# Performance work log

Measured on AMD Instinct MI355X. Metric: run time of the kernel, lower is better.

Reference implementation:

```python
import jax, jax.numpy as jnp
import numpy as np

N_NODES = 100000
N_EDGES = 1600000
N_GRAPHS = 256
F_IN = 54


def setup_inputs() -> dict:
    key = jax.random.key(0)
    ks = jax.random.split(key, 16)
    x = jax.random.normal(ks[0], (N_NODES, F_IN), dtype=jnp.float32)
    edge_index = jax.random.randint(ks[1], (2, N_EDGES), 0, N_NODES, dtype=jnp.int32)
    batch = jnp.sort(jax.random.randint(ks[2], (N_NODES,), 0, N_GRAPHS, dtype=jnp.int32))

    def lin(k, fi, fo):
        kw, kb = jax.random.split(k)
        lim = 1.0 / np.sqrt(fi)
        W = jax.random.uniform(kw, (fi, fo), minval=-lim, maxval=lim, dtype=jnp.float32)
        b = jax.random.uniform(kb, (fo,), minval=-lim, maxval=lim, dtype=jnp.float32)
        return W, b

    W1, b1 = lin(ks[3], 54, 54)
    W2, b2 = lin(ks[4], 54, 108)
    W3, b3 = lin(ks[5], 108, 216)
    Wf1, bf1 = lin(ks[6], 216, 1024)
    Wf2, bf2 = lin(ks[7], 1024, 128)
    return {"x": x, "edge_index": edge_index, "batch": batch,
            "W1": W1, "b1": b1, "W2": W2, "b2": b2, "W3": W3, "b3": b3,
            "Wf1": Wf1, "bf1": bf1, "Wf2": Wf2, "bf2": bf2}


def _gcn_norm(edge_index, n):
    # add self-loops, symmetric degree normalization (PyG GCNConv default)
    loop = jnp.arange(n, dtype=edge_index.dtype)
    row = jnp.concatenate([edge_index[0], loop])
    col = jnp.concatenate([edge_index[1], loop])
    deg = jax.ops.segment_sum(jnp.ones_like(col, dtype=jnp.float32), col, num_segments=n)
    dinv = jnp.where(deg > 0, jax.lax.rsqrt(deg), 0.0)
    norm = dinv[row] * dinv[col]
    return row, col, norm


def _gcn_conv(x, row, col, norm, W, b, n):
    h = x @ W                                  # [N, Fout]
    msg = h[row] * norm[:, None]               # [E+N, Fout] gather + scale
    out = jax.ops.segment_sum(msg, col, num_segments=n)  # scatter-add
    return out + b


def reference(x, edge_index, batch, W1, b1, W2, b2, W3, b3, Wf1, bf1, Wf2, bf2):
    n = x.shape[0]
    row, col, norm = _gcn_norm(edge_index, n)
    h = jax.nn.relu(_gcn_conv(x, row, col, norm, W1, b1, n))
    h = jax.nn.relu(_gcn_conv(h, row, col, norm, W2, b2, n))
    h = jax.nn.relu(_gcn_conv(h, row, col, norm, W3, b3, n))
    # global mean pool per graph
    sums = jax.ops.segment_sum(h, batch, num_segments=N_GRAPHS)
    cnts = jax.ops.segment_sum(jnp.ones((n,), jnp.float32), batch, num_segments=N_GRAPHS)
    pooled = sums / jnp.maximum(cnts, 1.0)[:, None]   # [G, 216]
    g = jax.nn.relu(pooled @ Wf1 + bf1)               # dropout = identity (eval)
    return g @ Wf2 + bf2                              # [G, 128]
```

## Files before the change

### kernel.cpp

```cpp
#include <hip/hip_runtime.h>


typedef _Float16 f16;
typedef _Float16 f16x2 __attribute__((ext_vector_type(2)));
typedef _Float16 f16x8 __attribute__((ext_vector_type(8)));
typedef float f32x4 __attribute__((ext_vector_type(4)));

static __host__ __device__ inline int cdiv(int a, int b) { return (a + b - 1) / b; }

constexpr int BSPAN = 512;
constexpr int EPB   = 4096;
constexpr int EPT   = EPB / 256;

template <int V>
__device__ __forceinline__ void vload(float* d, const float* s) {
    if constexpr (V == 1) { d[0] = s[0]; }
    else if constexpr (V == 2) { float2 t = *reinterpret_cast<const float2*>(s); d[0] = t.x; d[1] = t.y; }
    else { float4 t = *reinterpret_cast<const float4*>(s); d[0] = t.x; d[1] = t.y; d[2] = t.z; d[3] = t.w; }
}

__device__ __forceinline__ void wpack_one(const float* W, f16* Wb, int K, int F,
                                          int KT, int idx) {
    int j = idx & 7;
    int lane = (idx >> 3) & 63;
    int fi = idx >> 9;
    int kt = fi % KT;
    int nt = fi / KT;
    int k = kt * 32 + (lane >> 4) * 8 + j;
    int nn = nt * 16 + (lane & 15);
    Wb[idx] = (k < K && nn < F) ? (f16)W[k * F + nn] : (f16)0.f;
}

__global__ void k_init(const int* __restrict__ batch, int* __restrict__ start,
                       float* __restrict__ psum, int* __restrict__ bktCnt,
                       int* __restrict__ bktCur,
                       const float* __restrict__ W1, const float* __restrict__ W2,
                       const float* __restrict__ W3, f16* __restrict__ w1b,
                       f16* __restrict__ w2b, f16* __restrict__ w3b,
                       int n, int g) {
    int i = blockIdx.x * blockDim.x + threadIdx.x;
    if (i < g * 216) psum[i] = 0.f;
    if (i < 256) { bktCnt[i] = 0; bktCur[i] = 0; }
    constexpr int T1 = 4 * 2 * 512;
    constexpr int T2 = 7 * 2 * 512;
    constexpr int T3 = 14 * 4 * 512;
    if (i < T1) wpack_one(W1, w1b, 54, 54, 2, i);
    else if (i < T1 + T2) wpack_one(W2, w2b, 54, 108, 2, i - T1);
    else if (i < T1 + T2 + T3) wpack_one(W3, w3b, 108, 216, 4, i - T1 - T2);
    if (i < n) {
        int b = batch[i];
        int bp = (i == 0) ? -1 : batch[i - 1];
        for (int gg = bp + 1; gg <= b; gg++) start[gg] = i;
        if (i == n - 1)
            for (int gg = b + 1; gg <= g; gg++) start[gg] = n;
    }
}

__global__ __launch_bounds__(256) void k_bkt_hist(const int* __restrict__ col,
                                                  int* bktCnt, int e, int nb) {
    __shared__ int hist[256];
    int t = threadIdx.x;
    hist[t] = 0;
    __syncthreads();
    int base = blockIdx.x * EPB;
#pragma unroll
    for (int j = 0; j < EPT; j++) {
        int idx = base + j * 256 + t;
        if (idx < e) atomicAdd(&hist[col[idx] >> 9], 1);
    }
    __syncthreads();
    if (t < nb && hist[t] > 0) atomicAdd(&bktCnt[t], hist[t]);
}

__device__ __forceinline__ int scan256_ex(int* sbuf, int v, int t) {
    sbuf[t] = v;
    __syncthreads();
    for (int off = 1; off < 256; off <<= 1) {
        int x = sbuf[t];
        int y = (t >= off) ? sbuf[t - off] : 0;
        __syncthreads();
        sbuf[t] = x + y;
        __syncthreads();
    }
    return sbuf[t] - v;
}

__global__ __launch_bounds__(256) void k_bkt_part(const int* __restrict__ row,
                                                  const int* __restrict__ col,
                                                  const int* __restrict__ bktCnt,
                                                  int* bktCur, unsigned int* __restrict__ ebuf,
                                                  int e, int nb) {
    __shared__ int sbuf[256];
    __shared__ int hist[256];
    __shared__ int base[256];
    __shared__ int lcur[256];
    int t = threadIdx.x;
    int boff = scan256_ex(sbuf, (t < nb) ? bktCnt[t] : 0, t);
    hist[t] = 0; lcur[t] = 0;
    __syncthreads();
    int bs = blockIdx.x * EPB;
    unsigned int pk[EPT];
    int b[EPT];
#pragma unroll
    for (int j = 0; j < EPT; j++) {
        int idx = bs + j * 256 + t;
        if (idx < e) {
            int c = col[idx];
            pk[j] = ((unsigned int)(c & (BSPAN - 1)) << 17) | (unsigned int)row[idx];
            b[j] = c >> 9;
            atomicAdd(&hist[b[j]], 1);
        } else b[j] = -1;
    }
    __syncthreads();
    if (t < nb && hist[t] > 0) base[t] = boff + atomicAdd(&bktCur[t], hist[t]);
    __syncthreads();
#pragma unroll
    for (int j = 0; j < EPT; j++) {
        if (b[j] >= 0) {
            int lofs = atomicAdd(&lcur[b[j]], 1);
            ebuf[base[b[j]] + lofs] = pk[j];
        }
    }
}

__global__ __launch_bounds__(256) void k_bkt_build(const unsigned int* __restrict__ ebuf,
                                                   const int* __restrict__ bktCnt,
                                                   int* __restrict__ rowptr,
                                                   float* __restrict__ dinv,
                                                   int* __restrict__ eSrc,
                                                   int n, int nb) {
    __shared__ int sbuf[256];
    __shared__ int hist[BSPAN];
    __shared__ int cur[BSPAN];
    int t = threadIdx.x;
    int bkt = blockIdx.x;

    int boff_ex = scan256_ex(sbuf, (t < nb) ? bktCnt[t] : 0, t);
    __shared__ int boff_s, cnt_s;
    if (t == bkt) boff_s = boff_ex;
    if (t == 0) cnt_s = bktCnt[bkt];
    hist[t] = 0; hist[t + 256] = 0;
    __syncthreads();
    int es = boff_s, ee = boff_s + cnt_s;

    {
        int i = es + t;
        for (; i + 3 * 256 < ee; i += 4 * 256) {
            unsigned p0 = ebuf[i], p1 = ebuf[i + 256], p2 = ebuf[i + 512], p3 = ebuf[i + 768];
            atomicAdd(&hist[p0 >> 17], 1);
            atomicAdd(&hist[p1 >> 17], 1);
            atomicAdd(&hist[p2 >> 17], 1);
            atomicAdd(&hist[p3 >> 17], 1);
        }
        for (; i < ee; i += 256) atomicAdd(&hist[ebuf[i] >> 17], 1);
    }
    __syncthreads();

    int h0 = hist[2 * t], h1 = hist[2 * t + 1];
    __syncthreads();
    int ex = scan256_ex(sbuf, h0 + h1, t);
    int e0 = es + ex, e1 = e0 + h0;

    int node0 = bkt * BSPAN;
    int n0 = node0 + 2 * t, n1 = node0 + 2 * t + 1;
    if (n0 <= n) rowptr[n0] = e0;
    if (n1 <= n) rowptr[n1] = e1;
    if (n0 < n) dinv[n0] = rsqrtf((float)(h0 + 1));
    if (n1 < n) dinv[n1] = rsqrtf((float)(h1 + 1));
    cur[2 * t] = e0; cur[2 * t + 1] = e1;
    __syncthreads();

    {
        int i = es + t;
        for (; i + 3 * 256 < ee; i += 4 * 256) {
            unsigned p0 = ebuf[i], p1 = ebuf[i + 256], p2 = ebuf[i + 512], p3 = ebuf[i + 768];
            int s0 = atomicAdd(&cur[p0 >> 17], 1);
            int s1 = atomicAdd(&cur[p1 >> 17], 1);
            int s2 = atomicAdd(&cur[p2 >> 17], 1);
            int s3 = atomicAdd(&cur[p3 >> 17], 1);
            eSrc[s0] = (int)(p0 & 0x1FFFFu);
            eSrc[s1] = (int)(p1 & 0x1FFFFu);
            eSrc[s2] = (int)(p2 & 0x1FFFFu);
            eSrc[s3] = (int)(p3 & 0x1FFFFu);
        }
        for (; i < ee; i += 256) {
            unsigned int p = ebuf[i];
            int slot = atomicAdd(&cur[p >> 17], 1);
            eSrc[slot] = (int)(p & 0x1FFFFu);
        }
    }
}

template <int F, int RS>
__global__ void k_prescale(const float* __restrict__ x, const float* __restrict__ dinv,
                           f16* __restrict__ xs, int n) {
    constexpr int CH = F / 2;
    int idx = blockIdx.x * blockDim.x + threadIdx.x;
    if (idx >= n * CH) return;
    int node = idx / CH;
    int c = idx - node * CH;
    float d = dinv[node];
    float v[2];
    vload<2>(v, x + (long long)node * F + c * 2);
    f16x2 h;
    h[0] = (f16)(v[0] * d);
    h[1] = (f16)(v[1] * d);
    *reinterpret_cast<f16x2*>(xs + (long long)node * RS + c * 2) = h;
}

template <int F, int RS>
__global__ __launch_bounds__(256) void k_gatherw(
        const int* __restrict__ rowptr, const int* __restrict__ eSrc,
        const float* __restrict__ dinv, const f16* __restrict__ hs,
        f16* __restrict__ out, int n) {
    constexpr int CGN = RS / 8;
    constexpr int EPW = 64 / CGN;
    int wave = threadIdx.x >> 6;
    int lane = threadIdx.x & 63;
    int eslot = lane / CGN;
    int cg = lane & (CGN - 1);
    int node = blockIdx.x * 4 + wave;
    if (node >= n) return;
    int ch0 = cg * 8;
    int lim = F - ch0;
    if (lim > 8) lim = 8;
    if (lim < 0) lim = 0;

    int rs_ = rowptr[node], re = rowptr[node + 1];
    float di = dinv[node];
    int deg = re - rs_;
    int myidx = 0;
    if (lane < deg) myidx = eSrc[rs_ + lane];

    const f16x8* src = reinterpret_cast<const f16x8*>(hs);
    float acc[8];
#pragma unroll
    for (int j = 0; j < 8; j++) acc[j] = 0.f;

    if (eslot == 0) {
        f16x8 v = src[(long long)node * CGN + cg];
#pragma unroll
        for (int j = 0; j < 8; j++) acc[j] += (float)v[j];
    }

    int nfull = deg < 64 ? deg : 64;
    int base = 0;
    for (; base + 4 * EPW <= nfull; base += 4 * EPW) {
        int s0 = __shfl(myidx, base + eslot);
        int s1 = __shfl(myidx, base + EPW + eslot);
        int s2 = __shfl(myidx, base + 2 * EPW + eslot);
        int s3 = __shfl(myidx, base + 3 * EPW + eslot);
        f16x8 v0 = src[(long long)s0 * CGN + cg];
        f16x8 v1 = src[(long long)s1 * CGN + cg];
        f16x8 v2 = src[(long long)s2 * CGN + cg];
        f16x8 v3 = src[(long long)s3 * CGN + cg];
#pragma unroll
        for (int j = 0; j < 8; j++)
            acc[j] += ((float)v0[j] + (float)v1[j]) + ((float)v2[j] + (float)v3[j]);
    }
    for (; base + 2 * EPW <= nfull; base += 2 * EPW) {
        int s0 = __shfl(myidx, base + eslot);
        int s1 = __shfl(myidx, base + EPW + eslot);
        f16x8 v0 = src[(long long)s0 * CGN + cg];
        f16x8 v1 = src[(long long)s1 * CGN + cg];
#pragma unroll
        for (int j = 0; j < 8; j++) acc[j] += (float)v0[j] + (float)v1[j];
    }
    for (; base + EPW <= nfull; base += EPW) {
        int s = __shfl(myidx, base + eslot);
        f16x8 v = src[(long long)s * CGN + cg];
#pragma unroll
        for (int j = 0; j < 8; j++) acc[j] += (float)v[j];
    }
    if (base < nfull) {
        int idx = base + eslot;
        int s = __shfl(myidx, idx < 63 ? idx : 63);
        if (idx < nfull) {
            f16x8 v = src[(long long)s * CGN + cg];
#pragma unroll
            for (int j = 0; j < 8; j++) acc[j] += (float)v[j];
        }
    }
    for (int e = rs_ + 64 + eslot; e < re; e += EPW) {
        int s = eSrc[e];
        f16x8 v = src[(long long)s * CGN + cg];
#pragma unroll
        for (int j = 0; j < 8; j++) acc[j] += (float)v[j];
    }

#pragma unroll
    for (int j = 0; j < 8; j++)
        if (j >= lim) acc[j] = 0.f;
#pragma unroll
    for (int m = CGN; m < 64; m <<= 1)
#pragma unroll
        for (int j = 0; j < 8; j++) acc[j] += __shfl_xor(acc[j], m);

    if (eslot == 0) {
        f16x8 o;
#pragma unroll
        for (int j = 0; j < 8; j++) o[j] = (f16)(acc[j] * di);
        *reinterpret_cast<f16x8*>(out + (long long)node * RS + ch0) = o;
    }
}

template <int F, int KTILES, int NTILES, int FOUT, int OSTR>
__global__ __launch_bounds__(256) void k_gcn_fused(
        const int* __restrict__ rowptr, const int* __restrict__ eSrc,
        const float* __restrict__ dinv, const f16* __restrict__ hs,
        const f16* __restrict__ Wb, const float* __restrict__ bias,
        f16* __restrict__ outh, int n) {
    constexpr int KPAD = KTILES * 32;
    constexpr int KP   = KPAD + 8;
    constexpr int CGN  = KPAD / 8;
    constexpr int EPH  = 32 / CGN;

    __shared__ __align__(16) f16 a_lds[64 * KP];

    int t = threadIdx.x;
    int node0 = blockIdx.x * 64;
    int w = t >> 6;
    int lane = t & 63;
    int half = lane >> 5;
    int l = lane & 31;
    int eslot = l / CGN;
    int cg = l & (CGN - 1);
    int ch0 = cg * 8;
    int lim = F - ch0;
    if (lim > 8) lim = 8;
    if (lim < 0) lim = 0;
    int lbase = half * 32;

    const f16x8* src = reinterpret_cast<const f16x8*>(hs);
    int nodeBase = node0 + w * 16;

    for (int i = 0; i < 8; i++) {
        int node = nodeBase + 2 * i + half;
        float acc[8];
#pragma unroll
        for (int j = 0; j < 8; j++) acc[j] = 0.f;
        float di = 0.f;

        if (node < n) {
            int rs_ = rowptr[node], re = rowptr[node + 1];
            di = dinv[node];
            int deg = re - rs_;
            int myidx = 0;
            if (l < deg) myidx = eSrc[rs_ + l];

            if (eslot == 0) {
                f16x8 v = src[(long long)node * CGN + cg];
#pragma unroll
                for (int j = 0; j < 8; j++) acc[j] += (float)v[j];
            }

            int nfull = deg < 32 ? deg : 32;
            int base = 0;
            for (; base + 4 * EPH <= nfull; base += 4 * EPH) {
                int s0 = __shfl(myidx, lbase + base + eslot);
                int s1 = __shfl(myidx, lbase + base + EPH + eslot);
                int s2 = __shfl(myidx, lbase + base + 2 * EPH + eslot);
                int s3 = __shfl(myidx, lbase + base + 3 * EPH + eslot);
                f16x8 v0 = src[(long long)s0 * CGN + cg];
                f16x8 v1 = src[(long long)s1 * CGN + cg];
                f16x8 v2 = src[(long long)s2 * CGN + cg];
                f16x8 v3 = src[(long long)s3 * CGN + cg];
#pragma unroll
                for (int j = 0; j < 8; j++)
                    acc[j] += ((float)v0[j] + (float)v1[j]) + ((float)v2[j] + (float)v3[j]);
            }
            for (; base + 2 * EPH <= nfull; base += 2 * EPH) {
                int s0 = __shfl(myidx, lbase + base + eslot);
                int s1 = __shfl(myidx, lbase + base + EPH + eslot);
                f16x8 v0 = src[(long long)s0 * CGN + cg];
                f16x8 v1 = src[(long long)s1 * CGN + cg];
#pragma unroll
                for (int j = 0; j < 8; j++) acc[j] += (float)v0[j] + (float)v1[j];
            }
            for (; base + EPH <= nfull; base += EPH) {
                int s = __shfl(myidx, lbase + base + eslot);
                f16x8 v = src[(long long)s * CGN + cg];
#pragma unroll
                for (int j = 0; j < 8; j++) acc[j] += (float)v[j];
            }
            if (base < nfull) {
                int idx = base + eslot;
                int s = __shfl(myidx, lbase + (idx < 31 ? idx : 31));
                if (idx < nfull) {
                    f16x8 v = src[(long long)s * CGN + cg];
#pragma unroll
                    for (int j = 0; j < 8; j++) acc[j] += (float)v[j];
                }
            }
            for (int e = rs_ + 32 + eslot; e < re; e += EPH) {
                int s = eSrc[e];
                f16x8 v = src[(long long)s * CGN + cg];
#pragma unroll
                for (int j = 0; j < 8; j++) acc[j] += (float)v[j];
            }

#pragma unroll
            for (int j = 0; j < 8; j++)
                if (j >= lim) acc[j] = 0.f;
#pragma unroll
            for (int m = CGN; m < 32; m <<= 1)
#pragma unroll
                for (int j = 0; j < 8; j++) acc[j] += __shfl_xor(acc[j], m);
        }

        if (eslot == 0) {
            f16x8 o;
#pragma unroll
            for (int j = 0; j < 8; j++) o[j] = (f16)(acc[j] * di);
            *reinterpret_cast<f16x8*>(&a_lds[(w * 16 + 2 * i + half) * KP + ch0]) = o;
        }
    }
    __syncthreads();

    int quad = lane >> 4;
    int col = lane & 15;

    f16x8 afr[KTILES];
#pragma unroll
    for (int kt = 0; kt < KTILES; kt++)
        afr[kt] = *reinterpret_cast<const f16x8*>(
            &a_lds[(16 * w + col) * KP + kt * 32 + quad * 8]);

    int nodeC = node0 + 16 * w + quad * 4;
    float dv[4];
#pragma unroll
    for (int r = 0; r < 4; r++) {
        int nd = nodeC + r;
        dv[r] = (nd < n) ? dinv[nd] : 0.f;
    }

    const f16x8* wb = reinterpret_cast<const f16x8*>(Wb);
#pragma unroll
    for (int nt = 0; nt < NTILES; nt++) {
        f16x8 bfr[KTILES];
#pragma unroll
        for (int kt = 0; kt < KTILES; kt++)
            bfr[kt] = wb[(nt * KTILES + kt) * 64 + lane];
        f32x4 acc = {0.f, 0.f, 0.f, 0.f};
#pragma unroll
        for (int kt = 0; kt < KTILES; kt++)
            acc = __builtin_amdgcn_mfma_f32_16x16x32_f16(afr[kt], bfr[kt], acc, 0, 0, 0);

        int ch = nt * 16 + col;
        if (ch < FOUT) {
            float bval = bias[ch];
#pragma unroll
            for (int r = 0; r < 4; r++) {
                int nd = nodeC + r;
                if (nd < n)
                    outh[(long long)nd * OSTR + ch] =
                        (f16)(fmaxf(acc[r] + bval, 0.f) * dv[r]);
            }
        }
    }
}

template <int KTILES, int NTILES, int K, int FOUT>
__global__ __launch_bounds__(256) void k_gemm_pool(
        const f16* __restrict__ in, const f16* __restrict__ Wb,
        const float* __restrict__ bias, const int* __restrict__ batch,
        float* __restrict__ psum, int n) {
    constexpr int KPAD = KTILES * 32;
    constexpr int KP   = KPAD + 8;
    constexpr int V8   = KPAD / 8;
    constexpr int NSLOT = 4;

    __shared__ f16 a_lds[64 * KP];
    __shared__ float psum_l[NSLOT * FOUT];

    int t = threadIdx.x;
    int node0 = blockIdx.x * 64;

    const f16x8* inp = reinterpret_cast<const f16x8*>(in);
    for (int f = t; f < 64 * V8; f += 256) {
        int node = f / V8;
        int v = f - node * V8;
        f16x8 val = {};
        if (node0 + node < n) val = inp[(long long)(node0 + node) * V8 + v];
        *reinterpret_cast<f16x8*>(&a_lds[node * KP + v * 8]) = val;
    }
    for (int i = t; i < NSLOT * FOUT; i += 256) psum_l[i] = 0.f;
    __syncthreads();

    int w = t >> 6;
    int lane = t & 63;
    int quad = lane >> 4;
    int col = lane & 15;

    f16x8 afr[KTILES];
#pragma unroll
    for (int kt = 0; kt < KTILES; kt++)
        afr[kt] = *reinterpret_cast<const f16x8*>(
            &a_lds[(16 * w + col) * KP + kt * 32 + quad * 8]);

    int nodeC = node0 + 16 * w + quad * 4;
    int gb[4];
#pragma unroll
    for (int r = 0; r < 4; r++) {
        int nd = nodeC + r;
        gb[r] = (nd < n) ? batch[nd] : -1;
    }
    int g0 = batch[node0];

    const f16x8* wb = reinterpret_cast<const f16x8*>(Wb);
#pragma unroll
    for (int nt = 0; nt < NTILES; nt++) {
        f16x8 bfr[KTILES];
#pragma unroll
        for (int kt = 0; kt < KTILES; kt++)
            bfr[kt] = wb[(nt * KTILES + kt) * 64 + lane];
        f32x4 acc = {0.f, 0.f, 0.f, 0.f};
#pragma unroll
        for (int kt = 0; kt < KTILES; kt++)
            acc = __builtin_amdgcn_mfma_f32_16x16x32_f16(afr[kt], bfr[kt], acc, 0, 0, 0);

        int ch = nt * 16 + col;
        if (ch < FOUT) {
            float bval = bias[ch];
            if (gb[0] == gb[3] && gb[0] >= 0) {
                float s = fmaxf(acc[0] + bval, 0.f) + fmaxf(acc[1] + bval, 0.f)
                        + fmaxf(acc[2] + bval, 0.f) + fmaxf(acc[3] + bval, 0.f);
                int slot = gb[0] - g0;
                if (slot < NSLOT) atomicAdd(&psum_l[slot * FOUT + ch], s);
                else atomicAdd(&psum[gb[0] * FOUT + ch], s);
            } else {
#pragma unroll
                for (int r = 0; r < 4; r++) {
                    if (gb[r] < 0) continue;
                    float v = fmaxf(acc[r] + bval, 0.f);
                    int slot = gb[r] - g0;
                    if (slot < NSLOT) atomicAdd(&psum_l[slot * FOUT + ch], v);
                    else atomicAdd(&psum[gb[r] * FOUT + ch], v);
                }
            }
        }
    }

    __syncthreads();
    int lastNode = node0 + 63;
    if (lastNode >= n) lastNode = n - 1;
    int nsl = batch[lastNode] - g0 + 1;
    if (nsl > NSLOT) nsl = NSLOT;
    for (int f = t; f < nsl * FOUT; f += 256) {
        float v = psum_l[f];
        if (v != 0.f) atomicAdd(&psum[(g0 + f / FOUT) * FOUT + (f % FOUT)], v);
    }
}

__global__ void k_fc1(const float* __restrict__ P, const int* __restrict__ start,
                      const float* __restrict__ W, const float* __restrict__ bias,
                      float* __restrict__ out) {
    int row = blockIdx.x >> 2;
    int o = (blockIdx.x & 3) * 256 + threadIdx.x;
    int cnt = start[row + 1] - start[row];
    float scale = 1.0f / fmaxf((float)cnt, 1.0f);
    __shared__ float prow[216];
    if (threadIdx.x < 216) prow[threadIdx.x] = P[row * 216 + threadIdx.x] * scale;
    __syncthreads();
    float acc = bias[o];
    for (int k = 0; k < 216; k++) acc += prow[k] * W[k * 1024 + o];
    out[row * 1024 + o] = fmaxf(acc, 0.f);
}
__global__ void k_fc2(const float* __restrict__ G, const float* __restrict__ W,
                      const float* __restrict__ bias, float* __restrict__ out) {
    int row = blockIdx.x;
    int o = threadIdx.x;
    __shared__ float grow[1024];
    for (int k = threadIdx.x; k < 1024; k += 128) grow[k] = G[row * 1024 + k];
    __syncthreads();
    float acc = bias[o];
    for (int k = 0; k < 1024; k++) acc += grow[k] * W[k * 128 + o];
    out[row * 128 + o] = acc;
}

extern "C" void kernel_launch(void* const* d_in, const int* in_sizes, int n_in,
                              void* d_out, int out_size, void* d_ws, size_t ws_size,
                              hipStream_t stream) {
    const float* x     = (const float*)d_in[0];
    const int*   ei    = (const int*)d_in[1];
    const int*   batch = (const int*)d_in[2];
    const float* W1  = (const float*)d_in[3];
    const float* b1  = (const float*)d_in[4];
    const float* W2  = (const float*)d_in[5];
    const float* b2  = (const float*)d_in[6];
    const float* W3  = (const float*)d_in[7];
    const float* b3  = (const float*)d_in[8];
    const float* Wf1 = (const float*)d_in[9];
    const float* bf1 = (const float*)d_in[10];
    const float* Wf2 = (const float*)d_in[11];
    const float* bf2 = (const float*)d_in[12];
    float* out = (float*)d_out;

    const int N = in_sizes[0] / 54;
    const int E = in_sizes[1] / 2;
    const int G = 256;
    const int* row = ei;
    const int* col = ei + E;
    const int NB = cdiv(N, BSPAN);
    const int NBLK_A = cdiv(E, EPB);

    char* ws = (char*)d_ws;
    size_t off = 0;
    auto carve = [&](size_t bytes) {
        void* p = ws + off;
        off += (bytes + 255) & ~(size_t)255;
        return p;
    };
    int*   rowptr  = (int*)carve((size_t)(N + 1) * 4);
    int*   bktCnt  = (int*)carve(256 * 4);
    int*   bktCur  = (int*)carve(256 * 4);
    int*   eSrc    = (int*)carve((size_t)E * 4);
    float* dinv    = (float*)carve((size_t)N * 4);
    f16*   xs      = (f16*)carve((size_t)N * 64 * 2);
    f16*   hsbuf   = (f16*)carve((size_t)N * 128 * 2);
    f16*   bufA    = (f16*)carve((size_t)N * 128 * 2);
    unsigned int* ebuf = (unsigned int*)carve((size_t)E * 4);
    float* psum    = (float*)carve((size_t)G * 216 * 4);
    float* gbuf    = (float*)carve((size_t)G * 1024 * 4);
    int*   start   = (int*)carve((size_t)(G + 1) * 4);
    f16*   w1b     = (f16*)carve((size_t)4 * 2 * 512 * 2);
    f16*   w2b     = (f16*)carve((size_t)7 * 2 * 512 * 2);
    f16*   w3b     = (f16*)carve((size_t)14 * 4 * 512 * 2);

    const int T = 256;

    k_init<<<cdiv(N, T), T, 0, stream>>>(batch, start, psum, bktCnt, bktCur,
                                         W1, W2, W3, w1b, w2b, w3b, N, G);

    k_bkt_hist<<<NBLK_A, 256, 0, stream>>>(col, bktCnt, E, NB);
    k_bkt_part<<<NBLK_A, 256, 0, stream>>>(row, col, bktCnt, bktCur, ebuf, E, NB);
    k_bkt_build<<<NB, 256, 0, stream>>>(ebuf, bktCnt, rowptr, dinv, eSrc, N, NB);

    k_prescale<54, 64><<<cdiv(N * 27, T), T, 0, stream>>>(x, dinv, xs, N);

    const int GB = cdiv(N, 64);

    k_gcn_fused<54, 2, 4, 54, 64><<<GB, 256, 0, stream>>>(
        rowptr, eSrc, dinv, xs, w1b, b1, hsbuf, N);

    k_gcn_fused<54, 2, 7, 108, 128><<<GB, 256, 0, stream>>>(
        rowptr, eSrc, dinv, hsbuf, w2b, b2, bufA, N);

    k_gatherw<108, 128><<<cdiv(N, 4), 256, 0, stream>>>(rowptr, eSrc, dinv, bufA, hsbuf, N);
    k_gemm_pool<4, 14, 108, 216><<<GB, 256, 0, stream>>>(
        hsbuf, w3b, b3, batch, psum, N);

    k_fc1<<<G * 4, T, 0, stream>>>(psum, start, Wf1, bf1, gbuf);
    k_fc2<<<G, 128, 0, stream>>>(gbuf, Wf2, bf2, out);
}
```

Baseline: 385.7 us.

## Fuse bucket histogram into init, prescale into build; batch gather loads

```diff
diff --git a/kernel.cpp b/kernel.cpp
--- a/kernel.cpp
+++ b/kernel.cpp
@@ -11,13 +11,6 @@
 constexpr int BSPAN = 512;
 constexpr int EPB   = 4096;
 constexpr int EPT   = EPB / 256;
-
-template <int V>
-__device__ __forceinline__ void vload(float* d, const float* s) {
-    if constexpr (V == 1) { d[0] = s[0]; }
-    else if constexpr (V == 2) { float2 t = *reinterpret_cast<const float2*>(s); d[0] = t.x; d[1] = t.y; }
-    else { float4 t = *reinterpret_cast<const float4*>(s); d[0] = t.x; d[1] = t.y; d[2] = t.z; d[3] = t.w; }
-}
 
 __device__ __forceinline__ void wpack_one(const float* W, f16* Wb, int K, int F,
                                           int KT, int idx) {
@@ -31,16 +24,27 @@
     Wb[idx] = (k < K && nn < F) ? (f16)W[k * F + nn] : (f16)0.f;
 }
 
-__global__ void k_init(const int* __restrict__ batch, int* __restrict__ start,
-                       float* __restrict__ psum, int* __restrict__ bktCnt,
-                       int* __restrict__ bktCur,
-                       const float* __restrict__ W1, const float* __restrict__ W2,
-                       const float* __restrict__ W3, f16* __restrict__ w1b,
-                       f16* __restrict__ w2b, f16* __restrict__ w3b,
-                       int n, int g) {
-    int i = blockIdx.x * blockDim.x + threadIdx.x;
+__global__ __launch_bounds__(256) void k_init(
+        const int* __restrict__ batch, int* __restrict__ start,
+        float* __restrict__ psum, int* __restrict__ bktCnt, int* __restrict__ bktCur,
+        const int* __restrict__ col,
+        const float* __restrict__ W1, const float* __restrict__ W2,
+        const float* __restrict__ W3, f16* __restrict__ w1b,
+        f16* __restrict__ w2b, f16* __restrict__ w3b,
+        int e, int nb, int n, int g) {
+    __shared__ int hist[256];
+    int t = threadIdx.x;
+    int i = blockIdx.x * blockDim.x + t;
+    hist[t] = 0;
+    __syncthreads();
+    int ebase = blockIdx.x * EPB;
+#pragma unroll
+    for (int j = 0; j < EPT; j++) {
+        int idx = ebase + j * 256 + t;
+        if (idx < e) atomicAdd(&hist[col[idx] >> 9], 1);
+    }
     if (i < g * 216) psum[i] = 0.f;
-    if (i < 256) { bktCnt[i] = 0; bktCur[i] = 0; }
+    if (i < 256) bktCur[i] = 0;
     constexpr int T1 = 4 * 2 * 512;
     constexpr int T2 = 7 * 2 * 512;
     constexpr int T3 = 14 * 4 * 512;
@@ -54,20 +58,6 @@
         if (i == n - 1)
             for (int gg = b + 1; gg <= g; gg++) start[gg] = n;
     }
-}
-
-__global__ __launch_bounds__(256) void k_bkt_hist(const int* __restrict__ col,
-                                                  int* bktCnt, int e, int nb) {
-    __shared__ int hist[256];
-    int t = threadIdx.x;
-    hist[t] = 0;
-    __syncthreads();
-    int base = blockIdx.x * EPB;
-#pragma unroll
-    for (int j = 0; j < EPT; j++) {
-        int idx = base + j * 256 + t;
-        if (idx < e) atomicAdd(&hist[col[idx] >> 9], 1);
-    }
     __syncthreads();
     if (t < nb && hist[t] > 0) atomicAdd(&bktCnt[t], hist[t]);
 }
@@ -128,10 +118,13 @@
                                                    int* __restrict__ rowptr,
                                                    float* __restrict__ dinv,
                                                    int* __restrict__ eSrc,
+                                                   const float* __restrict__ x,
+                                                   f16* __restrict__ xs,
                                                    int n, int nb) {
     __shared__ int sbuf[256];
     __shared__ int hist[BSPAN];
     __shared__ int cur[BSPAN];
+    __shared__ float sdinv[BSPAN];
     int t = threadIdx.x;
     int bkt = blockIdx.x;
 
@@ -163,10 +156,12 @@
 
     int node0 = bkt * BSPAN;
     int n0 = node0 + 2 * t, n1 = node0 + 2 * t + 1;
+    float d0 = rsqrtf((float)(h0 + 1)), d1 = rsqrtf((float)(h1 + 1));
     if (n0 <= n) rowptr[n0] = e0;
     if (n1 <= n) rowptr[n1] = e1;
-    if (n0 < n) dinv[n0] = rsqrtf((float)(h0 + 1));
-    if (n1 < n) dinv[n1] = rsqrtf((float)(h1 + 1));
+    if (n0 < n) dinv[n0] = d0;
+    if (n1 < n) dinv[n1] = d1;
+    sdinv[2 * t] = d0; sdinv[2 * t + 1] = d1;
     cur[2 * t] = e0; cur[2 * t + 1] = e1;
     __syncthreads();
 
@@ -189,23 +184,20 @@
             eSrc[slot] = (int)(p & 0x1FFFFu);
         }
     }
-}
-
-template <int F, int RS>
-__global__ void k_prescale(const float* __restrict__ x, const float* __restrict__ dinv,
-                           f16* __restrict__ xs, int n) {
-    constexpr int CH = F / 2;
-    int idx = blockIdx.x * blockDim.x + threadIdx.x;
-    if (idx >= n * CH) return;
-    int node = idx / CH;
-    int c = idx - node * CH;
-    float d = dinv[node];
-    float v[2];
-    vload<2>(v, x + (long long)node * F + c * 2);
-    f16x2 h;
-    h[0] = (f16)(v[0] * d);
-    h[1] = (f16)(v[1] * d);
-    *reinterpret_cast<f16x2*>(xs + (long long)node * RS + c * 2) = h;
+
+    for (int idx = t; idx < BSPAN * 27; idx += 256) {
+        int nl = idx / 27;
+        int c = idx - nl * 27;
+        int node = node0 + nl;
+        if (node < n) {
+            float d = sdinv[nl];
+            float2 v = *reinterpret_cast<const float2*>(x + (long long)node * 54 + c * 2);
+            f16x2 h;
+            h[0] = (f16)(v.x * d);
+            h[1] = (f16)(v.y * d);
+            *reinterpret_cast<f16x2*>(xs + (long long)node * 64 + c * 2) = h;
+        }
+    }
 }
 
 template <int F, int RS>
@@ -244,41 +236,26 @@
     }
 
     int nfull = deg < 64 ? deg : 64;
-    int base = 0;
-    for (; base + 4 * EPW <= nfull; base += 4 * EPW) {
-        int s0 = __shfl(myidx, base + eslot);
-        int s1 = __shfl(myidx, base + EPW + eslot);
-        int s2 = __shfl(myidx, base + 2 * EPW + eslot);
-        int s3 = __shfl(myidx, base + 3 * EPW + eslot);
-        f16x8 v0 = src[(long long)s0 * CGN + cg];
-        f16x8 v1 = src[(long long)s1 * CGN + cg];
-        f16x8 v2 = src[(long long)s2 * CGN + cg];
-        f16x8 v3 = src[(long long)s3 * CGN + cg];
-#pragma unroll
-        for (int j = 0; j < 8; j++)
-            acc[j] += ((float)v0[j] + (float)v1[j]) + ((float)v2[j] + (float)v3[j]);
-    }
-    for (; base + 2 * EPW <= nfull; base += 2 * EPW) {
-        int s0 = __shfl(myidx, base + eslot);
-        int s1 = __shfl(myidx, base + EPW + eslot);
-        f16x8 v0 = src[(long long)s0 * CGN + cg];
-        f16x8 v1 = src[(long long)s1 * CGN + cg];
-#pragma unroll
-        for (int j = 0; j < 8; j++) acc[j] += (float)v0[j] + (float)v1[j];
-    }
-    for (; base + EPW <= nfull; base += EPW) {
-        int s = __shfl(myidx, base + eslot);
-        f16x8 v = src[(long long)s * CGN + cg];
-#pragma unroll
-        for (int j = 0; j < 8; j++) acc[j] += (float)v[j];
-    }
-    if (base < nfull) {
-        int idx = base + eslot;
-        int s = __shfl(myidx, idx < 63 ? idx : 63);
-        if (idx < nfull) {
-            f16x8 v = src[(long long)s * CGN + cg];
-#pragma unroll
-            for (int j = 0; j < 8; j++) acc[j] += (float)v[j];
+    for (int base = 0; base < nfull; base += 8 * EPW) {
+        int sidx[8];
+#pragma unroll
+        for (int u = 0; u < 8; u++) {
+            int idx = base + u * EPW + eslot;
+            sidx[u] = __shfl(myidx, idx < 63 ? idx : 63);
+        }
+        f16x8 v[8];
+#pragma unroll
+        for (int u = 0; u < 8; u++) {
+            int idx = base + u * EPW + eslot;
+            if (idx < nfull) v[u] = src[(long long)sidx[u] * CGN + cg];
+        }
+#pragma unroll
+        for (int u = 0; u < 8; u++) {
+            int idx = base + u * EPW + eslot;
+            if (idx < nfull) {
+#pragma unroll
+                for (int j = 0; j < 8; j++) acc[j] += (float)v[u][j];
+            }
         }
     }
     for (int e = rs_ + 64 + eslot; e < re; e += EPW) {
@@ -355,41 +332,26 @@
             }
 
             int nfull = deg < 32 ? deg : 32;
-            int base = 0;
-            for (; base + 4 * EPH <= nfull; base += 4 * EPH) {
-                int s0 = __shfl(myidx, lbase + base + eslot);
-                int s1 = __shfl(myidx, lbase + base + EPH + eslot);
-                int s2 = __shfl(myidx, lbase + base + 2 * EPH + eslot);
-                int s3 = __shfl(myidx, lbase + base + 3 * EPH + eslot);
-                f16x8 v0 = src[(long long)s0 * CGN + cg];
-                f16x8 v1 = src[(long long)s1 * CGN + cg];
-                f16x8 v2 = src[(long long)s2 * CGN + cg];
-                f16x8 v3 = src[(long long)s3 * CGN + cg];
-#pragma unroll
-                for (int j = 0; j < 8; j++)
-                    acc[j] += ((float)v0[j] + (float)v1[j]) + ((float)v2[j] + (float)v3[j]);
-            }
-            for (; base + 2 * EPH <= nfull; base += 2 * EPH) {
-                int s0 = __shfl(myidx, lbase + base + eslot);
-                int s1 = __shfl(myidx, lbase + base + EPH + eslot);
-                f16x8 v0 = src[(long long)s0 * CGN + cg];
-                f16x8 v1 = src[(long long)s1 * CGN + cg];
-#pragma unroll
-                for (int j = 0; j < 8; j++) acc[j] += (float)v0[j] + (float)v1[j];
-            }
-            for (; base + EPH <= nfull; base += EPH) {
-                int s = __shfl(myidx, lbase + base + eslot);
-                f16x8 v = src[(long long)s * CGN + cg];
-#pragma unroll
-                for (int j = 0; j < 8; j++) acc[j] += (float)v[j];
-            }
-            if (base < nfull) {
-                int idx = base + eslot;
-                int s = __shfl(myidx, lbase + (idx < 31 ? idx : 31));
-                if (idx < nfull) {
-                    f16x8 v = src[(long long)s * CGN + cg];
-#pragma unroll
-                    for (int j = 0; j < 8; j++) acc[j] += (float)v[j];
+            if (nfull > 0) {
+                int sidx[8];
+#pragma unroll
+                for (int u = 0; u < 8; u++) {
+                    int idx = u * EPH + eslot;
+                    sidx[u] = __shfl(myidx, lbase + (idx < 31 ? idx : 31));
+                }
+                f16x8 v[8];
+#pragma unroll
+                for (int u = 0; u < 8; u++) {
+                    int idx = u * EPH + eslot;
+                    if (idx < nfull) v[u] = src[(long long)sidx[u] * CGN + cg];
+                }
+#pragma unroll
+                for (int u = 0; u < 8; u++) {
+                    int idx = u * EPH + eslot;
+                    if (idx < nfull) {
+#pragma unroll
+                        for (int j = 0; j < 8; j++) acc[j] += (float)v[u][j];
+                    }
                 }
             }
             for (int e = rs_ + 32 + eslot; e < re; e += EPH) {
@@ -628,15 +590,14 @@
     f16*   w3b     = (f16*)carve((size_t)14 * 4 * 512 * 2);
 
     const int T = 256;
-
-    k_init<<<cdiv(N, T), T, 0, stream>>>(batch, start, psum, bktCnt, bktCur,
-                                         W1, W2, W3, w1b, w2b, w3b, N, G);
-
-    k_bkt_hist<<<NBLK_A, 256, 0, stream>>>(col, bktCnt, E, NB);
+    hipMemsetAsync(bktCnt, 0, 256 * 4, stream);
+
+    int gInit = cdiv(N, T) > NBLK_A ? cdiv(N, T) : NBLK_A;
+    k_init<<<gInit, T, 0, stream>>>(batch, start, psum, bktCnt, bktCur, col,
+                                    W1, W2, W3, w1b, w2b, w3b, E, NB, N, G);
+
     k_bkt_part<<<NBLK_A, 256, 0, stream>>>(row, col, bktCnt, bktCur, ebuf, E, NB);
-    k_bkt_build<<<NB, 256, 0, stream>>>(ebuf, bktCnt, rowptr, dinv, eSrc, N, NB);
-
-    k_prescale<54, 64><<<cdiv(N * 27, T), T, 0, stream>>>(x, dinv, xs, N);
+    k_bkt_build<<<NB, 256, 0, stream>>>(ebuf, bktCnt, rowptr, dinv, eSrc, x, xs, N, NB);
 
     const int GB = cdiv(N, 64);
 
```

Result: slower. 399.2 us (+3.5%).
